# Kernel tuning notes

Hardware: AMD Instinct MI355X
Metric: run time of the kernel (lower is better)

Reference implementation:

```python
import jax, jax.numpy as jnp
import numpy as np

B, T, S, H, E = 128, 32, 256, 1024, 1024


def setup_inputs() -> dict:
    key = jax.random.key(0)
    ks = jax.random.split(key, 8)
    sc = lambda n: 1.0 / np.sqrt(n)
    return dict(
        dec_seq=jax.random.normal(ks[0], (B, T, E), jnp.float32),      # embedded decoder inputs
        enc_hiddens=jax.random.normal(ks[1], (B, S, H), jnp.float32),  # encoder outputs
        last_hidden=jax.random.normal(ks[2], (B, H), jnp.float32),     # initial decoder state
        W_att=jax.random.normal(ks[3], (2 * H, H), jnp.float32) * sc(2 * H),  # concat-score W
        V_att=jax.random.normal(ks[4], (H, 1), jnp.float32) * sc(H),          # concat-score V
        Wi=jax.random.normal(ks[5], (E + H, 3 * H), jnp.float32) * sc(E + H),  # GRU input kernel (z,r,h)
        Uh=jax.random.normal(ks[6], (H, 3 * H), jnp.float32) * sc(H),          # GRU recurrent kernel
        b=jnp.zeros((3 * H,), jnp.float32),                                    # GRU bias
    )


def reference(dec_seq, enc_hiddens, last_hidden, W_att, V_att, Wi, Uh, b):
    Bn, Sn, Hn = enc_hiddens.shape

    def step(h, x_t):
        # Bahdanau 'concat' score: tanh([h; enc] @ W) @ V -> softmax over source
        hid = jnp.broadcast_to(h[:, None, :], (Bn, Sn, Hn))
        combined = jnp.concatenate([hid, enc_hiddens], axis=2)          # [B,S,2H]
        score = jnp.tanh(jnp.einsum('bsk,kh->bsh', combined, W_att))    # [B,S,H]
        score = jnp.einsum('bsh,h->bs', score, V_att[:, 0])             # [B,S]
        attn = jax.nn.softmax(score, axis=-1)
        context = jnp.einsum('bs,bsh->bh', attn, enc_hiddens)           # [B,H]
        # GRU cell on concat([x_t, context])
        inp = jnp.concatenate([x_t, context], axis=1)                   # [B,E+H]
        gz, gr, gh = jnp.split(inp @ Wi + b, 3, axis=1)
        rz, rr, rh = jnp.split(h @ Uh, 3, axis=1)
        z = jax.nn.sigmoid(gz + rz)
        r = jax.nn.sigmoid(gr + rr)
        hh = jnp.tanh(gh + r * rh)
        h_new = z * h + (1.0 - z) * hh
        return h_new, h_new

    _, outs = jax.lax.scan(step, last_hidden, jnp.swapaxes(dec_seq, 0, 1))
    return jnp.swapaxes(outs, 0, 1)  # [B,T,H]
```

## Files before the change

kernel.cpp:

```cpp
#include <hip/hip_runtime.h>
#include <hip/hip_bf16.h>
#include <stdint.h>

#define B_ 128
#define T_ 32
#define S_ 256
#define H_ 1024
#define E_ 1024
#define LOG2E 1.4426950408889634f

typedef __attribute__((ext_vector_type(8))) short short8;
typedef __attribute__((ext_vector_type(4))) float f32x4;

typedef const __attribute__((address_space(1))) unsigned int* gas_ptr;
typedef __attribute__((address_space(3))) unsigned int* las_ptr;

__device__ __forceinline__ void gl_lds16(const void* g, void* l) {
    __builtin_amdgcn_global_load_lds((gas_ptr)g, (las_ptr)l, 16, 0, 0);
}

__device__ __forceinline__ float bf2f(unsigned short u) {
    union { unsigned int i; float f; } v; v.i = ((unsigned int)u) << 16; return v.f;
}
__device__ __forceinline__ unsigned short f2bf(float f) {
    union { float f; unsigned int i; } v; v.f = f;
    unsigned int i = v.i;
    return (unsigned short)((i + 0x7FFFu + ((i >> 16) & 1u)) >> 16);
}
__device__ __forceinline__ float fexp2(float x) { return __builtin_amdgcn_exp2f(x); }
__device__ __forceinline__ float frcp(float x)  { return __builtin_amdgcn_rcpf(x); }
__device__ __forceinline__ float fast_tanh(float x) {
    float e = fexp2(x * (2.0f * LOG2E));
    return 1.0f - 2.0f * frcp(e + 1.0f);
}
__device__ __forceinline__ float fast_sigmoid(float x) {
    return frcp(1.0f + fexp2(-LOG2E * x));
}

__global__ __launch_bounds__(256) void conv_bf16(const float* __restrict__ src,
                                                 unsigned short* __restrict__ dst, long n) {
    long i = ((long)blockIdx.x * 256 + threadIdx.x) * 8;
    if (i >= n) return;
    float4 x = *(const float4*)(src + i);
    float4 y = *(const float4*)(src + i + 4);
    unsigned int w0 = (unsigned int)f2bf(x.x) | ((unsigned int)f2bf(x.y) << 16);
    unsigned int w1 = (unsigned int)f2bf(x.z) | ((unsigned int)f2bf(x.w) << 16);
    unsigned int w2 = (unsigned int)f2bf(y.x) | ((unsigned int)f2bf(y.y) << 16);
    unsigned int w3 = (unsigned int)f2bf(y.z) | ((unsigned int)f2bf(y.w) << 16);
    uint4 o; o.x = w0; o.y = w1; o.z = w2; o.w = w3;
    *(uint4*)(dst + i) = o;
}

__global__ __launch_bounds__(256) void init_h(const float* __restrict__ h0,
                                              float* __restrict__ hbuf,
                                              unsigned short* __restrict__ hbf, int n) {
    int i = blockIdx.x * 256 + threadIdx.x;
    if (i < n) { float v = h0[i]; hbuf[i] = v; hbf[i] = f2bf(v); }
}

__global__ __launch_bounds__(256) void transpose_conv(const float* __restrict__ src, int ldsrc,
                                                      unsigned short* __restrict__ dst, int lddst,
                                                      float scale) {
    __shared__ float tile[64][65];
    int tid = threadIdx.x;
    int c0 = blockIdx.x * 64, r0 = blockIdx.y * 64;
    int tr = tid >> 6, tc = tid & 63;
#pragma unroll
    for (int i = 0; i < 16; i++) {
        int r = i * 4 + tr;
        tile[r][tc] = src[(long)(r0 + r) * ldsrc + c0 + tc];
    }
    __syncthreads();
#pragma unroll
    for (int i = 0; i < 16; i++) {
        int rr = i * 4 + tr;
        dst[(long)(c0 + rr) * lddst + r0 + tc] = f2bf(scale * tile[tc][rr]);
    }
}

template <int EPIL, int SWZ>
__global__ __launch_bounds__(256) void gemm128(const unsigned short* __restrict__ A, int lda,
                                               const unsigned short* __restrict__ Bt, int ldb,
                                               void* __restrict__ Cout, int ldc,
                                               int kLen, long partStride) {
    __shared__ unsigned short As[128 * 32];
    __shared__ unsigned short Bs[128 * 32];
    const int tid = threadIdx.x;
    int lin = blockIdx.y * gridDim.x + blockIdx.x;
    if (SWZ) {
        int cpx = (gridDim.x * gridDim.y) >> 3;
        lin = (lin & 7) * cpx + (lin >> 3);
    }
    const int n0 = (lin % gridDim.x) * 128;
    const int m0 = (lin / gridDim.x) * 128;
    const int kStart = blockIdx.z * kLen;
    const int w = tid >> 6, l = tid & 63;
    const int wr = w >> 1, wc = w & 1;

    f32x4 acc[4][4];
#pragma unroll
    for (int i = 0; i < 4; i++)
#pragma unroll
        for (int j = 0; j < 4; j++) acc[i][j] = f32x4{0.f, 0.f, 0.f, 0.f};

    for (int kt = 0; kt < kLen; kt += 32) {
        int k0 = kStart + kt;
#pragma unroll
        for (int i = 0; i < 2; i++) {
            int f = i * 4096 + tid * 16;
            int row = f >> 6;
            int cb = f & 63;
            gl_lds16(A + (long)(m0 + row) * lda + k0 + (cb >> 1), (char*)As + f);
            gl_lds16(Bt + (long)(n0 + row) * ldb + k0 + (cb >> 1), (char*)Bs + f);
        }
        asm volatile("s_waitcnt vmcnt(0)" ::: "memory");
        __syncthreads();
        short8 a[4], b[4];
#pragma unroll
        for (int fi = 0; fi < 4; fi++) {
            a[fi] = *(const short8*)((const char*)As + ((wr * 64 + fi * 16 + (l & 15)) * 32 + ((l >> 4) * 8)) * 2);
            b[fi] = *(const short8*)((const char*)Bs + ((wc * 64 + fi * 16 + (l & 15)) * 32 + ((l >> 4) * 8)) * 2);
        }
#pragma unroll
        for (int fi = 0; fi < 4; fi++)
#pragma unroll
            for (int fj = 0; fj < 4; fj++)
                acc[fi][fj] = __builtin_amdgcn_mfma_f32_16x16x32_bf16(a[fi], b[fj], acc[fi][fj], 0, 0, 0);
        __syncthreads();
    }

    long cz = (long)blockIdx.z * partStride;
#pragma unroll
    for (int fi = 0; fi < 4; fi++)
#pragma unroll
        for (int fj = 0; fj < 4; fj++) {
            int m = m0 + wr * 64 + fi * 16 + ((l >> 4) << 2);
            int n = n0 + wc * 64 + fj * 16 + (l & 15);
#pragma unroll
            for (int r = 0; r < 4; r++) {
                if (EPIL == 0)
                    ((unsigned short*)Cout)[(long)(m + r) * ldc + n] = f2bf(acc[fi][fj][r]);
                else
                    ((float*)Cout + cz)[(long)(m + r) * ldc + n] = acc[fi][fj][r];
            }
        }
}

__global__ __launch_bounds__(256) void recgates(const unsigned short* __restrict__ hbf,
                                                const unsigned short* __restrict__ ctxbf,
                                                const unsigned short* __restrict__ Uht,
                                                const unsigned short* __restrict__ Wit2,
                                                float* __restrict__ gpart) {
    __shared__ unsigned short As[128 * 32];
    __shared__ unsigned short Bs[128 * 32];
    const int tid = threadIdx.x;
    const int n0 = blockIdx.x * 128;
    const int y = blockIdx.y, z = blockIdx.z;
    const unsigned short* A  = y ? ctxbf : hbf;
    const unsigned short* Bt = y ? Wit2 : Uht;
    const int kStart = z * 256;
    const int w = tid >> 6, l = tid & 63;
    const int wr = w >> 1, wc = w & 1;

    f32x4 acc[4][4];
#pragma unroll
    for (int i = 0; i < 4; i++)
#pragma unroll
        for (int j = 0; j < 4; j++) acc[i][j] = f32x4{0.f, 0.f, 0.f, 0.f};

    for (int kt = 0; kt < 256; kt += 32) {
        int k0 = kStart + kt;
#pragma unroll
        for (int i = 0; i < 2; i++) {
            int f = i * 4096 + tid * 16;
            int row = f >> 6;
            int cb = f & 63;
            gl_lds16(A + (long)row * 1024 + k0 + (cb >> 1), (char*)As + f);
            gl_lds16(Bt + (long)(n0 + row) * 1024 + k0 + (cb >> 1), (char*)Bs + f);
        }
        asm volatile("s_waitcnt vmcnt(0)" ::: "memory");
        __syncthreads();
        short8 a[4], b[4];
#pragma unroll
        for (int fi = 0; fi < 4; fi++) {
            a[fi] = *(const short8*)((const char*)As + ((wr * 64 + fi * 16 + (l & 15)) * 32 + ((l >> 4) * 8)) * 2);
            b[fi] = *(const short8*)((const char*)Bs + ((wc * 64 + fi * 16 + (l & 15)) * 32 + ((l >> 4) * 8)) * 2);
        }
#pragma unroll
        for (int fi = 0; fi < 4; fi++)
#pragma unroll
            for (int fj = 0; fj < 4; fj++)
                acc[fi][fj] = __builtin_amdgcn_mfma_f32_16x16x32_bf16(a[fi], b[fj], acc[fi][fj], 0, 0, 0);
        __syncthreads();
    }

    float* C = gpart + (long)(y * 4 + z) * (128 * 3072);
#pragma unroll
    for (int fi = 0; fi < 4; fi++)
#pragma unroll
        for (int fj = 0; fj < 4; fj++) {
            int m = wr * 64 + fi * 16 + ((l >> 4) << 2);
            int n = n0 + wc * 64 + fj * 16 + (l & 15);
#pragma unroll
            for (int r = 0; r < 4; r++)
                C[(long)(m + r) * 3072 + n] = acc[fi][fj][r];
        }
}

__global__ __launch_bounds__(256) void attn_kernel(const unsigned short* __restrict__ P,
                                                   const unsigned short* __restrict__ encbf,
                                                   const float* __restrict__ partq,
                                                   const float* __restrict__ V,
                                                   float* __restrict__ pctx,
                                                   float* __restrict__ pml) {
    const int oct = blockIdx.x, b = blockIdx.y;
    const int tid = threadIdx.x, w = tid >> 6, l = tid & 63;
    __shared__ float qs[1024];
    __shared__ float sc[32];
    __shared__ float wgt[32];

    {
        int j = tid * 4;
        float s0 = 0.f, s1 = 0.f, s2 = 0.f, s3 = 0.f;
#pragma unroll
        for (int p = 0; p < 8; p++) {
            const float* pp = partq + (long)p * (128 * 1024) + (long)b * 1024 + j;
            float4 v = *(const float4*)pp;
            s0 += v.x; s1 += v.y; s2 += v.z; s3 += v.w;
        }
        qs[j] = s0; qs[j + 1] = s1; qs[j + 2] = s2; qs[j + 3] = s3;
    }
    __syncthreads();

    float q[16], nv2[16];
    float sv = 0.f;
#pragma unroll
    for (int ii = 0; ii < 4; ii++) {
        float4 qq = *(const float4*)(qs + l * 16 + ii * 4);
        float4 vv = *(const float4*)(V + l * 16 + ii * 4);
        q[ii * 4 + 0] = qq.x; q[ii * 4 + 1] = qq.y; q[ii * 4 + 2] = qq.z; q[ii * 4 + 3] = qq.w;
        nv2[ii * 4 + 0] = -2.f * vv.x; nv2[ii * 4 + 1] = -2.f * vv.y;
        nv2[ii * 4 + 2] = -2.f * vv.z; nv2[ii * 4 + 3] = -2.f * vv.w;
        sv += vv.x + vv.y + vv.z + vv.w;
    }

    const int s0 = oct * 32;
#pragma unroll 2
    for (int ss = 0; ss < 8; ss++) {
        int s = w * 8 + ss;
        const unsigned short* prow = P + ((long)(b * S_ + s0 + s)) * H_ + l * 16;
        short8 pa = *(const short8*)prow;
        short8 pb = *(const short8*)(prow + 8);
        float acc = sv;
#pragma unroll
        for (int i = 0; i < 8; i++) {
            float x = q[i] + bf2f((unsigned short)pa[i]);
            float d = frcp(fexp2(x) + 1.0f);
            acc = fmaf(d, nv2[i], acc);
        }
#pragma unroll
        for (int i = 0; i < 8; i++) {
            float x = q[8 + i] + bf2f((unsigned short)pb[i]);
            float d = frcp(fexp2(x) + 1.0f);
            acc = fmaf(d, nv2[8 + i], acc);
        }
#pragma unroll
        for (int off = 32; off; off >>= 1) acc += __shfl_xor(acc, off);
        if (l == 0) sc[s] = acc;
    }
    __syncthreads();

    float v = (l < 32) ? sc[l] : -3.4e38f;
    float mx = v;
#pragma unroll
    for (int off = 32; off; off >>= 1) mx = fmaxf(mx, __shfl_xor(mx, off));
    float ex = (l < 32) ? fexp2((v - mx) * LOG2E) : 0.f;
    float ls = ex;
#pragma unroll
    for (int off = 32; off; off >>= 1) ls += __shfl_xor(ls, off);
    if (tid < 32) wgt[tid] = ex;
    if (tid == 0) {
        pml[(oct * 128 + b) * 2 + 0] = mx;
        pml[(oct * 128 + b) * 2 + 1] = ls;
    }
    __syncthreads();

    float a0 = 0.f, a1 = 0.f, a2 = 0.f, a3 = 0.f;
    const unsigned short* ebase = encbf + ((long)(b * S_ + s0)) * H_ + tid * 4;
#pragma unroll 4
    for (int s = 0; s < 32; s++) {
        float ws = wgt[s];
        ushort4 e = *(const ushort4*)(ebase + (long)s * H_);
        a0 = fmaf(ws, bf2f(e.x), a0);
        a1 = fmaf(ws, bf2f(e.y), a1);
        a2 = fmaf(ws, bf2f(e.z), a2);
        a3 = fmaf(ws, bf2f(e.w), a3);
    }
    float* po = pctx + ((long)(oct * 128 + b)) * H_ + tid * 4;
    po[0] = a0; po[1] = a1; po[2] = a2; po[3] = a3;
}

__global__ __launch_bounds__(256) void combine_ctx(const float* __restrict__ pctx,
                                                   const float* __restrict__ pml,
                                                   unsigned short* __restrict__ ctxbf) {
    int b = blockIdx.x, tid = threadIdx.x;
    float mm[8], ll[8];
    float m = -3.4e38f;
#pragma unroll
    for (int p = 0; p < 8; p++) {
        mm[p] = pml[(p * 128 + b) * 2 + 0];
        ll[p] = pml[(p * 128 + b) * 2 + 1];
        m = fmaxf(m, mm[p]);
    }
    float denom = 0.f, f[8];
#pragma unroll
    for (int p = 0; p < 8; p++) { f[p] = fexp2((mm[p] - m) * LOG2E); denom += f[p] * ll[p]; }
    float inv = frcp(denom);
    float a0 = 0.f, a1 = 0.f, a2 = 0.f, a3 = 0.f;
#pragma unroll
    for (int p = 0; p < 8; p++) {
        float4 c = *(const float4*)(pctx + ((long)(p * 128 + b)) * H_ + tid * 4);
        a0 = fmaf(f[p], c.x, a0); a1 = fmaf(f[p], c.y, a1);
        a2 = fmaf(f[p], c.z, a2); a3 = fmaf(f[p], c.w, a3);
    }
    unsigned short* o = ctxbf + (long)b * H_ + tid * 4;
    o[0] = f2bf(a0 * inv); o[1] = f2bf(a1 * inv); o[2] = f2bf(a2 * inv); o[3] = f2bf(a3 * inv);
}

__global__ __launch_bounds__(256) void gru_update(const float* __restrict__ gpart,
                                                  const unsigned short* __restrict__ xg,
                                                  const float* __restrict__ bias,
                                                  float* __restrict__ hbuf,
                                                  unsigned short* __restrict__ hbf,
                                                  float* __restrict__ out, int t) {
    const int m = blockIdx.x;
    const int j = threadIdx.x * 4;
    const unsigned short* xr = xg + ((long)(m * T_ + t)) * 3072;
    ushort4 xz = *(const ushort4*)(xr + j);
    ushort4 xrr = *(const ushort4*)(xr + 1024 + j);
    ushort4 xh = *(const ushort4*)(xr + 2048 + j);
    float gz[4] = {bf2f(xz.x), bf2f(xz.y), bf2f(xz.z), bf2f(xz.w)};
    float gr[4] = {bf2f(xrr.x), bf2f(xrr.y), bf2f(xrr.z), bf2f(xrr.w)};
    float gh[4] = {bf2f(xh.x), bf2f(xh.y), bf2f(xh.z), bf2f(xh.w)};
    float rz[4] = {0, 0, 0, 0}, rr[4] = {0, 0, 0, 0}, rh[4] = {0, 0, 0, 0};
#pragma unroll
    for (int p = 0; p < 8; p++) {
        const float* gp = gpart + (long)p * (128 * 3072) + (long)m * 3072;
        float4 a = *(const float4*)(gp + j);
        float4 bb = *(const float4*)(gp + 1024 + j);
        float4 c = *(const float4*)(gp + 2048 + j);
        if (p < 4) {
            rz[0] += a.x; rz[1] += a.y; rz[2] += a.z; rz[3] += a.w;
            rr[0] += bb.x; rr[1] += bb.y; rr[2] += bb.z; rr[3] += bb.w;
            rh[0] += c.x; rh[1] += c.y; rh[2] += c.z; rh[3] += c.w;
        } else {
            gz[0] += a.x; gz[1] += a.y; gz[2] += a.z; gz[3] += a.w;
            gr[0] += bb.x; gr[1] += bb.y; gr[2] += bb.z; gr[3] += bb.w;
            gh[0] += c.x; gh[1] += c.y; gh[2] += c.z; gh[3] += c.w;
        }
    }
    float4 bz = *(const float4*)(bias + j);
    float4 br = *(const float4*)(bias + 1024 + j);
    float4 bh = *(const float4*)(bias + 2048 + j);
    float4 hv = *(const float4*)(hbuf + (long)m * H_ + j);
    float bzf[4] = {bz.x, bz.y, bz.z, bz.w};
    float brf[4] = {br.x, br.y, br.z, br.w};
    float bhf[4] = {bh.x, bh.y, bh.z, bh.w};
    float hf[4] = {hv.x, hv.y, hv.z, hv.w};
    float hn[4];
    ushort4 hb;
#pragma unroll
    for (int c = 0; c < 4; c++) {
        float z = fast_sigmoid(gz[c] + bzf[c] + rz[c]);
        float r = fast_sigmoid(gr[c] + brf[c] + rr[c]);
        float hh = fast_tanh(gh[c] + bhf[c] + r * rh[c]);
        hn[c] = z * hf[c] + (1.0f - z) * hh;
    }
    hb.x = f2bf(hn[0]); hb.y = f2bf(hn[1]); hb.z = f2bf(hn[2]); hb.w = f2bf(hn[3]);
    float4 ho; ho.x = hn[0]; ho.y = hn[1]; ho.z = hn[2]; ho.w = hn[3];
    *(float4*)(out + ((long)m * T_ + t) * H_ + j) = ho;
    *(float4*)(hbuf + (long)m * H_ + j) = ho;
    *(ushort4*)(hbf + (long)m * H_ + j) = hb;
}

__global__ void sentinel_k(float* out) {
    if (threadIdx.x == 0 && blockIdx.x == 0) out[0] = 1.2345e8f;
}

extern "C" void kernel_launch(void* const* d_in, const int* in_sizes, int n_in,
                              void* d_out, int out_size, void* d_ws, size_t ws_size,
                              hipStream_t stream) {
    const float* dec  = (const float*)d_in[0];
    const float* enc  = (const float*)d_in[1];
    const float* h0   = (const float*)d_in[2];
    const float* Watt = (const float*)d_in[3];
    const float* Vatt = (const float*)d_in[4];
    const float* Wi   = (const float*)d_in[5];
    const float* Uh   = (const float*)d_in[6];
    const float* bias = (const float*)d_in[7];
    float* out = (float*)d_out;

    char* ws = (char*)d_ws;
    size_t off = 0;
    auto alloc = [&](size_t bytes) -> void* {
        void* p = ws + off;
        off += (bytes + 255) & ~(size_t)255;
        return p;
    };
    unsigned short* P     = (unsigned short*)alloc((size_t)32768 * 1024 * 2);
    unsigned short* encbf = (unsigned short*)alloc((size_t)33554432 * 2);
    unsigned short* decbf = (unsigned short*)alloc((size_t)4194304 * 2);
    unsigned short* Xg    = (unsigned short*)alloc((size_t)4096 * 3072 * 2);
    unsigned short* Wit1  = (unsigned short*)alloc((size_t)3072 * 1024 * 2);
    unsigned short* Wit2  = (unsigned short*)alloc((size_t)3072 * 1024 * 2);
    unsigned short* Uht   = (unsigned short*)alloc((size_t)3072 * 1024 * 2);
    unsigned short* W1t   = (unsigned short*)alloc((size_t)1024 * 1024 * 2);
    unsigned short* W2t   = (unsigned short*)alloc((size_t)1024 * 1024 * 2);
    float* partq = (float*)alloc((size_t)8 * 128 * 1024 * 4);
    float* gpart = (float*)alloc((size_t)8 * 128 * 3072 * 4);
    float* pctx  = (float*)alloc((size_t)8 * 128 * 1024 * 4);
    float* pml   = (float*)alloc((size_t)8 * 128 * 2 * 4);
    unsigned short* ctxbf = (unsigned short*)alloc((size_t)128 * 1024 * 2);
    float* hbuf  = (float*)alloc((size_t)128 * 1024 * 4);
    unsigned short* hbf = (unsigned short*)alloc((size_t)128 * 1024 * 2);

    if (off > ws_size) {
        sentinel_k<<<1, 64, 0, stream>>>(out);
        return;
    }

    const float qscale = 2.0f * LOG2E;

    conv_bf16<<<33554432 / 8 / 256, 256, 0, stream>>>(enc, encbf, 33554432);
    conv_bf16<<<4194304 / 8 / 256, 256, 0, stream>>>(dec, decbf, 4194304);
    init_h<<<512, 256, 0, stream>>>(h0, hbuf, hbf, 131072);
    transpose_conv<<<dim3(48, 16), 256, 0, stream>>>(Wi, 3072, Wit1, 1024, 1.0f);
    transpose_conv<<<dim3(48, 16), 256, 0, stream>>>(Wi + (size_t)1024 * 3072, 3072, Wit2, 1024, 1.0f);
    transpose_conv<<<dim3(48, 16), 256, 0, stream>>>(Uh, 3072, Uht, 1024, 1.0f);
    transpose_conv<<<dim3(16, 16), 256, 0, stream>>>(Watt, 1024, W1t, 1024, qscale);
    transpose_conv<<<dim3(16, 16), 256, 0, stream>>>(Watt + (size_t)1024 * 1024, 1024, W2t, 1024, qscale);
    gemm128<0, 1><<<dim3(8, 256, 1), 256, 0, stream>>>(encbf, 1024, W2t, 1024, P, 1024, 1024, 0);
    gemm128<0, 1><<<dim3(24, 32, 1), 256, 0, stream>>>(decbf, 1024, Wit1, 1024, Xg, 3072, 1024, 0);

    for (int t = 0; t < T_; t++) {
        gemm128<1, 0><<<dim3(8, 1, 8), 256, 0, stream>>>(hbf, 1024, W1t, 1024, partq, 1024, 128,
                                                         (long)128 * 1024);
        attn_kernel<<<dim3(8, 128), 256, 0, stream>>>(P, encbf, partq, Vatt, pctx, pml);
        combine_ctx<<<128, 256, 0, stream>>>(pctx, pml, ctxbf);
        recgates<<<dim3(24, 2, 4), 256, 0, stream>>>(hbf, ctxbf, Uht, Wit2, gpart);
        gru_update<<<128, 256, 0, stream>>>(gpart, Xg, bias, hbuf, hbf, out, t);
    }
}
```

Measured before the change: 1.737 ms.

## Store attention key projection in FP8 and fuse context combine into attention kernel

The precomputed encoder projection P is now stored as FP8 instead of bf16, which halves the bytes the per-step attention kernel streams on each of the 32 timesteps. The separate combine_ctx launch is removed. The last block per batch row, found through an atomic counter, does the softmax merge and writes the bf16 context. This costs extra quantization error in the attention scores and adds atomic and threadfence synchronization.

```diff
diff --git a/kernel.cpp b/kernel.cpp
--- a/kernel.cpp
+++ b/kernel.cpp
@@ -11,6 +11,7 @@
 
 typedef __attribute__((ext_vector_type(8))) short short8;
 typedef __attribute__((ext_vector_type(4))) float f32x4;
+typedef __attribute__((ext_vector_type(2))) float f32x2;
 
 typedef const __attribute__((address_space(1))) unsigned int* gas_ptr;
 typedef __attribute__((address_space(3))) unsigned int* las_ptr;
@@ -53,9 +54,11 @@
 
 __global__ __launch_bounds__(256) void init_h(const float* __restrict__ h0,
                                               float* __restrict__ hbuf,
-                                              unsigned short* __restrict__ hbf, int n) {
+                                              unsigned short* __restrict__ hbf,
+                                              int* __restrict__ cnt, int n) {
     int i = blockIdx.x * 256 + threadIdx.x;
     if (i < n) { float v = h0[i]; hbuf[i] = v; hbf[i] = f2bf(v); }
+    if (i < 128) cnt[i] = 0;
 }
 
 __global__ __launch_bounds__(256) void transpose_conv(const float* __restrict__ src, int ldsrc,
@@ -140,8 +143,13 @@
             for (int r = 0; r < 4; r++) {
                 if (EPIL == 0)
                     ((unsigned short*)Cout)[(long)(m + r) * ldc + n] = f2bf(acc[fi][fj][r]);
-                else
+                else if (EPIL == 1)
                     ((float*)Cout + cz)[(long)(m + r) * ldc + n] = acc[fi][fj][r];
+                else {
+                    float v = acc[fi][fj][r];
+                    unsigned int pk = (unsigned int)__builtin_amdgcn_cvt_pk_fp8_f32(v, v, 0, false);
+                    ((unsigned char*)Cout)[(long)(m + r) * ldc + n] = (unsigned char)(pk & 0xFF);
+                }
             }
         }
 }
@@ -207,17 +215,20 @@
         }
 }
 
-__global__ __launch_bounds__(256) void attn_kernel(const unsigned short* __restrict__ P,
+__global__ __launch_bounds__(256) void attn_kernel(const unsigned char* __restrict__ P8,
                                                    const unsigned short* __restrict__ encbf,
                                                    const float* __restrict__ partq,
                                                    const float* __restrict__ V,
                                                    float* __restrict__ pctx,
-                                                   float* __restrict__ pml) {
+                                                   float* __restrict__ pml,
+                                                   unsigned short* __restrict__ ctxbf,
+                                                   int* __restrict__ cnt) {
     const int oct = blockIdx.x, b = blockIdx.y;
     const int tid = threadIdx.x, w = tid >> 6, l = tid & 63;
     __shared__ float qs[1024];
     __shared__ float sc[32];
     __shared__ float wgt[32];
+    __shared__ int lastFlag;
 
     {
         int j = tid * 4;
@@ -248,21 +259,26 @@
 #pragma unroll 2
     for (int ss = 0; ss < 8; ss++) {
         int s = w * 8 + ss;
-        const unsigned short* prow = P + ((long)(b * S_ + s0 + s)) * H_ + l * 16;
-        short8 pa = *(const short8*)prow;
-        short8 pb = *(const short8*)(prow + 8);
+        const unsigned char* prow = P8 + ((long)(b * S_ + s0 + s)) * H_ + l * 16;
+        uint4 pw = *(const uint4*)prow;
+        float pv[16];
+        {
+            f32x2 d;
+            d = __builtin_amdgcn_cvt_pk_f32_fp8(pw.x, false); pv[0] = d.x; pv[1] = d.y;
+            d = __builtin_amdgcn_cvt_pk_f32_fp8(pw.x, true);  pv[2] = d.x; pv[3] = d.y;
+            d = __builtin_amdgcn_cvt_pk_f32_fp8(pw.y, false); pv[4] = d.x; pv[5] = d.y;
+            d = __builtin_amdgcn_cvt_pk_f32_fp8(pw.y, true);  pv[6] = d.x; pv[7] = d.y;
+            d = __builtin_amdgcn_cvt_pk_f32_fp8(pw.z, false); pv[8] = d.x; pv[9] = d.y;
+            d = __builtin_amdgcn_cvt_pk_f32_fp8(pw.z, true);  pv[10] = d.x; pv[11] = d.y;
+            d = __builtin_amdgcn_cvt_pk_f32_fp8(pw.w, false); pv[12] = d.x; pv[13] = d.y;
+            d = __builtin_amdgcn_cvt_pk_f32_fp8(pw.w, true);  pv[14] = d.x; pv[15] = d.y;
+        }
         float acc = sv;
 #pragma unroll
-        for (int i = 0; i < 8; i++) {
-            float x = q[i] + bf2f((unsigned short)pa[i]);
+        for (int i = 0; i < 16; i++) {
+            float x = q[i] + pv[i];
             float d = frcp(fexp2(x) + 1.0f);
             acc = fmaf(d, nv2[i], acc);
-        }
-#pragma unroll
-        for (int i = 0; i < 8; i++) {
-            float x = q[8 + i] + bf2f((unsigned short)pb[i]);
-            float d = frcp(fexp2(x) + 1.0f);
-            acc = fmaf(d, nv2[8 + i], acc);
         }
 #pragma unroll
         for (int off = 32; off; off >>= 1) acc += __shfl_xor(acc, off);
@@ -298,33 +314,39 @@
     }
     float* po = pctx + ((long)(oct * 128 + b)) * H_ + tid * 4;
     po[0] = a0; po[1] = a1; po[2] = a2; po[3] = a3;
-}
-
-__global__ __launch_bounds__(256) void combine_ctx(const float* __restrict__ pctx,
-                                                   const float* __restrict__ pml,
-                                                   unsigned short* __restrict__ ctxbf) {
-    int b = blockIdx.x, tid = threadIdx.x;
-    float mm[8], ll[8];
-    float m = -3.4e38f;
-#pragma unroll
-    for (int p = 0; p < 8; p++) {
-        mm[p] = pml[(p * 128 + b) * 2 + 0];
-        ll[p] = pml[(p * 128 + b) * 2 + 1];
-        m = fmaxf(m, mm[p]);
-    }
-    float denom = 0.f, f[8];
-#pragma unroll
-    for (int p = 0; p < 8; p++) { f[p] = fexp2((mm[p] - m) * LOG2E); denom += f[p] * ll[p]; }
-    float inv = frcp(denom);
-    float a0 = 0.f, a1 = 0.f, a2 = 0.f, a3 = 0.f;
-#pragma unroll
-    for (int p = 0; p < 8; p++) {
-        float4 c = *(const float4*)(pctx + ((long)(p * 128 + b)) * H_ + tid * 4);
-        a0 = fmaf(f[p], c.x, a0); a1 = fmaf(f[p], c.y, a1);
-        a2 = fmaf(f[p], c.z, a2); a3 = fmaf(f[p], c.w, a3);
-    }
-    unsigned short* o = ctxbf + (long)b * H_ + tid * 4;
-    o[0] = f2bf(a0 * inv); o[1] = f2bf(a1 * inv); o[2] = f2bf(a2 * inv); o[3] = f2bf(a3 * inv);
+
+    __threadfence();
+    __syncthreads();
+    if (tid == 0) {
+        int old = atomicAdd(&cnt[b], 1);
+        lastFlag = (old == 7);
+    }
+    __syncthreads();
+    if (lastFlag) {
+        __threadfence();
+        float mm[8], ll[8], m = -3.4e38f;
+#pragma unroll
+        for (int p = 0; p < 8; p++) {
+            mm[p] = pml[(p * 128 + b) * 2 + 0];
+            ll[p] = pml[(p * 128 + b) * 2 + 1];
+            m = fmaxf(m, mm[p]);
+        }
+        float denom = 0.f, f[8];
+#pragma unroll
+        for (int p = 0; p < 8; p++) { f[p] = fexp2((mm[p] - m) * LOG2E); denom += f[p] * ll[p]; }
+        float inv = frcp(denom);
+        int j = tid * 4;
+        float c0 = 0.f, c1 = 0.f, c2 = 0.f, c3 = 0.f;
+#pragma unroll
+        for (int p = 0; p < 8; p++) {
+            float4 c = *(const float4*)(pctx + ((long)(p * 128 + b)) * H_ + j);
+            c0 = fmaf(f[p], c.x, c0); c1 = fmaf(f[p], c.y, c1);
+            c2 = fmaf(f[p], c.z, c2); c3 = fmaf(f[p], c.w, c3);
+        }
+        unsigned short* o = ctxbf + (long)b * H_ + j;
+        o[0] = f2bf(c0 * inv); o[1] = f2bf(c1 * inv); o[2] = f2bf(c2 * inv); o[3] = f2bf(c3 * inv);
+        if (tid == 0) cnt[b] = 0;
+    }
 }
 
 __global__ __launch_bounds__(256) void gru_update(const float* __restrict__ gpart,
@@ -407,7 +429,7 @@
         off += (bytes + 255) & ~(size_t)255;
         return p;
     };
-    unsigned short* P     = (unsigned short*)alloc((size_t)32768 * 1024 * 2);
+    unsigned char*  P8    = (unsigned char*)alloc((size_t)32768 * 1024);
     unsigned short* encbf = (unsigned short*)alloc((size_t)33554432 * 2);
     unsigned short* decbf = (unsigned short*)alloc((size_t)4194304 * 2);
     unsigned short* Xg    = (unsigned short*)alloc((size_t)4096 * 3072 * 2);
@@ -420,6 +442,7 @@
     float* gpart = (float*)alloc((size_t)8 * 128 * 3072 * 4);
     float* pctx  = (float*)alloc((size_t)8 * 128 * 1024 * 4);
     float* pml   = (float*)alloc((size_t)8 * 128 * 2 * 4);
+    int*   cnt   = (int*)alloc((size_t)128 * 4);
     unsigned short* ctxbf = (unsigned short*)alloc((size_t)128 * 1024 * 2);
     float* hbuf  = (float*)alloc((size_t)128 * 1024 * 4);
     unsigned short* hbf = (unsigned short*)alloc((size_t)128 * 1024 * 2);
@@ -433,20 +456,19 @@
 
     conv_bf16<<<33554432 / 8 / 256, 256, 0, stream>>>(enc, encbf, 33554432);
     conv_bf16<<<4194304 / 8 / 256, 256, 0, stream>>>(dec, decbf, 4194304);
-    init_h<<<512, 256, 0, stream>>>(h0, hbuf, hbf, 131072);
+    init_h<<<512, 256, 0, stream>>>(h0, hbuf, hbf, cnt, 131072);
     transpose_conv<<<dim3(48, 16), 256, 0, stream>>>(Wi, 3072, Wit1, 1024, 1.0f);
     transpose_conv<<<dim3(48, 16), 256, 0, stream>>>(Wi + (size_t)1024 * 3072, 3072, Wit2, 1024, 1.0f);
     transpose_conv<<<dim3(48, 16), 256, 0, stream>>>(Uh, 3072, Uht, 1024, 1.0f);
     transpose_conv<<<dim3(16, 16), 256, 0, stream>>>(Watt, 1024, W1t, 1024, qscale);
     transpose_conv<<<dim3(16, 16), 256, 0, stream>>>(Watt + (size_t)1024 * 1024, 1024, W2t, 1024, qscale);
-    gemm128<0, 1><<<dim3(8, 256, 1), 256, 0, stream>>>(encbf, 1024, W2t, 1024, P, 1024, 1024, 0);
+    gemm128<2, 1><<<dim3(8, 256, 1), 256, 0, stream>>>(encbf, 1024, W2t, 1024, P8, 1024, 1024, 0);
     gemm128<0, 1><<<dim3(24, 32, 1), 256, 0, stream>>>(decbf, 1024, Wit1, 1024, Xg, 3072, 1024, 0);
 
     for (int t = 0; t < T_; t++) {
         gemm128<1, 0><<<dim3(8, 1, 8), 256, 0, stream>>>(hbf, 1024, W1t, 1024, partq, 1024, 128,
                                                          (long)128 * 1024);
-        attn_kernel<<<dim3(8, 128), 256, 0, stream>>>(P, encbf, partq, Vatt, pctx, pml);
-        combine_ctx<<<128, 256, 0, stream>>>(pctx, pml, ctxbf);
+        attn_kernel<<<dim3(8, 128), 256, 0, stream>>>(P8, encbf, partq, Vatt, pctx, pml, ctxbf, cnt);
         recgates<<<dim3(24, 2, 4), 256, 0, stream>>>(hbf, ctxbf, Uht, Wit2, gpart);
         gru_update<<<128, 256, 0, stream>>>(gpart, Xg, bias, hbuf, hbf, out, t);
     }
```

New measurement: 5.975 ms. 244% more time.
